# Optimization experiments

Measured on AMD Instinct MI355X. Metric: run time of the kernel, lower is better.

Reference implementation:

```python
import jax, jax.numpy as jnp
import numpy as np
from itertools import combinations_with_replacement

B, T, F, L, POLY_ORDER = 16, 2048, 128, 16, 3


def _hilbert_filter(N):
    # Matches pytorch_hilbert: H[0]=0, H[1:N//2]=2, H[N//2]=0 (even N)
    h = np.zeros(N, dtype=np.float32)
    if N % 2 == 0:
        h[1:N // 2] = 2.0
    else:
        h[1:(N + 1) // 2] = 2.0
    return jnp.asarray(h)


def hilbert(sig, axis=1):
    N = sig.shape[axis]
    Xf = jnp.fft.fft(sig, axis=axis)
    shape = [1] * sig.ndim
    shape[axis] = N
    return jnp.fft.ifft(Xf * _hilbert_filter(N).reshape(shape), axis=axis)


def _combo_indices(latent, poly_order):
    # static index arrays, grouped by degree n
    return [np.array(list(combinations_with_replacement(range(latent), n)), dtype=np.int32)
            for n in range(1, poly_order + 1)]


def compute_library(z, poly_order):
    # z: [B, T, L] -> theta: [B, T, library_dim]
    feats = []
    for combos in _combo_indices(z.shape[-1], poly_order):
        zc = z[..., combos]            # [B, T, ncomb, n]
        feats.append(jnp.prod(zc, axis=-1))  # [B, T, ncomb]
    analytic = hilbert(z, axis=1)
    feats.append(z)
    feats.append(jnp.abs(analytic))    # extract_real_component
    feats.append(jnp.angle(analytic))  # extract_imaginary_component
    return jnp.concatenate(feats, axis=-1)


def setup_inputs() -> dict:
    key = jax.random.key(0)
    ks = jax.random.split(key, 7)
    lib_dim = L + 2 * L + sum(len(c) for c in _combo_indices(L, POLY_ORDER))
    s_enc = 1.0 / np.sqrt(F)
    s_dec = 1.0 / np.sqrt(L)
    s_sin = 1.0 / np.sqrt(lib_dim)
    return {
        "x": jax.random.normal(ks[0], (B, T, F), dtype=jnp.float32),
        "W_enc": jax.random.uniform(ks[1], (L, F), jnp.float32, -s_enc, s_enc),
        "b_enc": jax.random.uniform(ks[2], (L,), jnp.float32, -s_enc, s_enc),
        "W_dec": jax.random.uniform(ks[3], (F, L), jnp.float32, -s_dec, s_dec),
        "b_dec": jax.random.uniform(ks[4], (F,), jnp.float32, -s_dec, s_dec),
        "W_sindy": jax.random.uniform(ks[5], (L, lib_dim), jnp.float32, -s_sin, s_sin),
        "b_sindy": jax.random.uniform(ks[6], (L,), jnp.float32, -s_sin, s_sin),
    }


def reference(x, W_enc, b_enc, W_dec, b_dec, W_sindy, b_sindy):
    z = jnp.einsum('btf,lf->btl', x, W_enc) + b_enc          # encoder
    theta = compute_library(z, POLY_ORDER)                    # [B,T,lib_dim]
    y_hat = jnp.einsum('btd,ld->btl', theta, W_sindy) + b_sindy
    x_hat = jnp.einsum('btl,fl->btf', z, W_dec) + b_dec       # decoder
    # Jacobian of the linear encoder w.r.t. x is the constant weight matrix
    # broadcast per (b, t): identical math to the O((B*T)^2) autograd version.
    jac_z_x = jnp.broadcast_to(W_enc, (x.shape[0], x.shape[1], L, F))
    return (y_hat, x_hat, z, jac_z_x, W_sindy, W_dec)
```

## Files before the change

kernel.cpp:

```cpp
#include <hip/hip_runtime.h>
#include <math.h>

typedef unsigned short u16;
typedef unsigned int   u32;
typedef __attribute__((ext_vector_type(4))) float f32x4;

#define OFF_AT    0
#define OFF_PT    524288
#define OFF_WT    1048576
#define OFF_ZT    1064832
#define OFF_TWC   1589120
#define OFF_TWS   1591168

#define R1_LO 0
#define R1_HI 5592576
#define R2_LO 5592576
#define R2_HI 11185152
#define R3_LO 11185152
#define R3_HI 16777216

__device__ __forceinline__ void jac_range(const float* __restrict__ Wenc,
                                          float* __restrict__ out_jac,
                                          int lo, int hi, int idx, int nth)
{
    const float* wsrc = Wenc + (size_t)((lo + idx) & 511) * 4;
    f32x4 w;
    w.x = wsrc[0]; w.y = wsrc[1]; w.z = wsrc[2]; w.w = wsrc[3];
    f32x4* j4 = (f32x4*)out_jac;
    for (int i = lo + idx; i < hi; i += nth)
        __builtin_nontemporal_store(w, j4 + i);
}

__global__ __launch_bounds__(256) void k1_encdec(
    const float* __restrict__ x, const float* __restrict__ Wenc, const float* __restrict__ benc,
    const float* __restrict__ Wdec, const float* __restrict__ bdec,
    const float* __restrict__ Wsin,
    float* __restrict__ out_z, float* __restrict__ out_xhat,
    float* __restrict__ out_Ws, float* __restrict__ out_Wd,
    float* __restrict__ z_t, float* __restrict__ wt,
    double* __restrict__ twc_g, double* __restrict__ tws_g,
    float* __restrict__ out_jac)
{
    int tid = threadIdx.x;
    int blk = blockIdx.x;

    if (blk >= 2116) {
        jac_range(Wenc, out_jac, R1_LO, R1_HI, (blk - 2116) * 256 + tid, 262144);
        return;
    }
    if (blk >= 2048) {
        int t0 = (blk - 2048) * 256 + tid;
        if (t0 < 16256) {
            float v = Wsin[t0];
            out_Ws[t0] = v;
            int l = t0 / 1016;
            int d = t0 - l * 1016;
            if (d < 16) v += Wsin[t0 + 968];
            wt[d * 16 + l] = v;
        } else if (t0 < 17280) {
            int k = t0 - 16256;
            double ang = -6.283185307179586476925286766559 * (double)k / 2048.0;
            double s_, c_;
            sincos(ang, &s_, &c_);
            twc_g[k] = c_;
            tws_g[k] = s_;
        }
        if (t0 < 2048) out_Wd[t0] = Wdec[t0];
        return;
    }

    __shared__ float xs[16][128];
    __shared__ float we[16][132];
    __shared__ float wd[128][17];
    __shared__ float zs[16][16];

    {
        const float4* xv = (const float4*)x + (size_t)blk * 512;
        float* dst = &xs[0][0];
        float4 a = xv[tid], b = xv[tid + 256];
        dst[tid*4+0]=a.x; dst[tid*4+1]=a.y; dst[tid*4+2]=a.z; dst[tid*4+3]=a.w;
        dst[(tid+256)*4+0]=b.x; dst[(tid+256)*4+1]=b.y; dst[(tid+256)*4+2]=b.z; dst[(tid+256)*4+3]=b.w;
    }
    {
        const float4* wev = (const float4*)Wenc;
        #pragma unroll
        for (int h = 0; h < 2; ++h) {
            int vi = tid + h * 256;
            float4 v = wev[vi];
            int base = vi * 4, row = base >> 7, col = base & 127;
            we[row][col+0]=v.x; we[row][col+1]=v.y; we[row][col+2]=v.z; we[row][col+3]=v.w;
        }
    }
    {
        const float4* wdv = (const float4*)Wdec;
        #pragma unroll
        for (int h = 0; h < 2; ++h) {
            int vi = tid + h * 256;
            float4 v = wdv[vi];
            int base = vi * 4, row = base >> 4, col = base & 15;
            wd[row][col+0]=v.x; wd[row][col+1]=v.y; wd[row][col+2]=v.z; wd[row][col+3]=v.w;
        }
    }
    __syncthreads();

    {
        int r = tid >> 4, l = tid & 15;
        float s = 0.f;
        #pragma unroll 8
        for (int f = 0; f < 128; ++f) s += xs[r][f] * we[l][f];
        float zv = s + benc[l];
        zs[r][l] = zv;
        out_z[blk * 256 + tid] = zv;
    }
    __syncthreads();

    {
        int l2 = tid >> 4, r2 = tid & 15;
        z_t[l2 * 32768 + blk * 16 + r2] = zs[r2][l2];
    }

    #pragma unroll
    for (int u = 0; u < 8; ++u) {
        int idx = u * 256 + tid;
        int rr = idx >> 7, f = idx & 127;
        float acc = bdec[f];
        #pragma unroll
        for (int ll = 0; ll < 16; ++ll) acc += zs[rr][ll] * wd[f][ll];
        out_xhat[(size_t)blk * 2048 + idx] = acc;
    }
}

#define TWPAD(k) ((k) + ((k) >> 5))
#define CP(i)    ((i) + ((i) >> 4))

__global__ __launch_bounds__(1024) void k2_hilbert(
    const float* __restrict__ z_t, const double* __restrict__ twc_g,
    const double* __restrict__ tws_g, const float* __restrict__ Wenc,
    float* __restrict__ a_t, float* __restrict__ p_t,
    float* __restrict__ out_jac)
{
    __shared__ double2 c[2176];
    __shared__ double twc_s[1056];
    __shared__ double tws_s[1056];

    int tid = threadIdx.x;
    if (blockIdx.x >= 256) {
        jac_range(Wenc, out_jac, R2_LO, R2_HI, (blockIdx.x - 256) * 1024 + tid, 524288);
        return;
    }
    int b = blockIdx.x >> 4, l = blockIdx.x & 15;
    const size_t base = (size_t)l * 32768 + (size_t)b * 2048;
    const float* zp = z_t + base;

    {
        twc_s[TWPAD(tid)] = twc_g[tid];
        tws_s[TWPAD(tid)] = tws_g[tid];
    }
    {
        double2 v0; v0.x = (double)zp[tid];        v0.y = 0.0;
        double2 v1; v1.x = (double)zp[tid + 1024]; v1.y = 0.0;
        c[CP(tid)] = v0;
        c[CP(tid + 1024)] = v1;
    }
    __syncthreads();

    for (int half = 1024; half >= 1; half >>= 1) {
        int step = 1024 / half;
        int j = tid & (half - 1);
        int pos = ((tid - j) << 1) + j;
        int pa = CP(pos), pb = CP(pos + half);
        int ti = TWPAD(j * step);
        double2 u = c[pa], v = c[pb];
        double wc = twc_s[ti], wsn = tws_s[ti];
        double2 s, dsc;
        s.x = u.x + v.x;  s.y = u.y + v.y;
        double br = u.x - v.x, bi = u.y - v.y;
        dsc.x = br * wc - bi * wsn;
        dsc.y = br * wsn + bi * wc;
        c[pa] = s;
        c[pb] = dsc;
        __syncthreads();
    }

    #pragma unroll
    for (int h = 0; h < 2; ++h) {
        int t = tid + h * 1024;
        double sc = (t == 0 || (t & 1)) ? 0.0 : (2.0 / 2048.0);
        int ci = CP(t);
        double2 v = c[ci];
        v.x *= sc; v.y *= sc;
        c[ci] = v;
    }
    __syncthreads();

    for (int half = 1; half <= 1024; half <<= 1) {
        int step = 1024 / half;
        int j = tid & (half - 1);
        int pos = ((tid - j) << 1) + j;
        int pa = CP(pos), pb = CP(pos + half);
        int ti = TWPAD(j * step);
        double2 u = c[pa], v = c[pb];
        double wc = twc_s[ti], wsn = tws_s[ti];
        double tr = v.x * wc + v.y * wsn;
        double ti2 = v.y * wc - v.x * wsn;
        double2 p0, p1;
        p0.x = u.x + tr; p0.y = u.y + ti2;
        p1.x = u.x - tr; p1.y = u.y - ti2;
        c[pa] = p0;
        c[pb] = p1;
        __syncthreads();
    }

    #pragma unroll
    for (int h = 0; h < 2; ++h) {
        int t = tid + h * 1024;
        double2 v = c[CP(t)];
        a_t[base + t] = (float)sqrt(v.x * v.x + v.y * v.y);
        p_t[base + t] = (float)atan2(v.y, v.x);
    }
}

#define EMIT2(EXPR) do {                                                    \
    if ((unsigned)(d - LO) < 121u) {                                        \
        float vv[2];                                                        \
        _Pragma("unroll") for (int p = 0; p < 2; ++p) vv[p] = (EXPR);       \
        int bb = (d - LO) << 4;                                             \
        _Pragma("unroll") for (int l = 0; l < 16; ++l) {                    \
            float w = lw[bb + l];                                           \
            acc[0][l] = fmaf(vv[0], w, acc[0][l]);                          \
            acc[1][l] = fmaf(vv[1], w, acc[1][l]);                          \
        }                                                                   \
    }                                                                       \
    ++d;                                                                    \
} while (0)

template<int LO>
__device__ __forceinline__ void poly_accum(const float (&z)[2][16],
                                           const float* __restrict__ lw,
                                           float (&acc)[2][16])
{
    int d = 0;
    #pragma unroll
    for (int i = 0; i < 16; ++i) EMIT2(z[p][i]);
    #pragma unroll
    for (int i = 0; i < 16; ++i)
        #pragma unroll
        for (int j = i; j < 16; ++j) EMIT2(z[p][i] * z[p][j]);
    #pragma unroll
    for (int i = 0; i < 16; ++i)
        #pragma unroll
        for (int j = i; j < 16; ++j)
            #pragma unroll
            for (int k = j; k < 16; ++k) EMIT2(z[p][i] * z[p][j] * z[p][k]);
}

__global__ __launch_bounds__(256, 2) void k3_yhat(
    const float* __restrict__ z_ws, const float* __restrict__ wt,
    const float* __restrict__ Wenc,
    float* __restrict__ part, float* __restrict__ out_jac)
{
    __shared__ float lw[1936];
    int tid = threadIdx.x;
    if (blockIdx.x >= 512) {
        jac_range(Wenc, out_jac, R3_LO, R3_HI, (blockIdx.x - 512) * 256 + tid, 262144);
        return;
    }
    int slice = blockIdx.x >> 6;
    int ptgrp = blockIdx.x & 63;
    int base = ptgrp * 512;

    {
        const float4* src = (const float4*)(wt + slice * 121 * 16);
        float4* dst = (float4*)lw;
        for (int i = tid; i < 484; i += 256) dst[i] = src[i];
    }
    __syncthreads();

    float z[2][16], acc[2][16];
    #pragma unroll
    for (int p = 0; p < 2; ++p) {
        int bt = base + p * 256 + tid;
        const float4* zp = (const float4*)(z_ws + (size_t)bt * 16);
        #pragma unroll
        for (int q = 0; q < 4; ++q) {
            float4 v = zp[q];
            z[p][q*4+0]=v.x; z[p][q*4+1]=v.y; z[p][q*4+2]=v.z; z[p][q*4+3]=v.w;
        }
    }
    #pragma unroll
    for (int p = 0; p < 2; ++p)
        #pragma unroll
        for (int l = 0; l < 16; ++l) acc[p][l] = 0.f;

    switch (slice) {
        case 0: poly_accum<0 * 121>(z, lw, acc); break;
        case 1: poly_accum<1 * 121>(z, lw, acc); break;
        case 2: poly_accum<2 * 121>(z, lw, acc); break;
        case 3: poly_accum<3 * 121>(z, lw, acc); break;
        case 4: poly_accum<4 * 121>(z, lw, acc); break;
        case 5: poly_accum<5 * 121>(z, lw, acc); break;
        case 6: poly_accum<6 * 121>(z, lw, acc); break;
        default: poly_accum<7 * 121>(z, lw, acc); break;
    }

    #pragma unroll
    for (int p = 0; p < 2; ++p) {
        int bt = base + p * 256 + tid;
        float4* pp = (float4*)(part + (size_t)slice * 524288 + (size_t)bt * 16);
        #pragma unroll
        for (int q = 0; q < 4; ++q) {
            float4 v;
            v.x = acc[p][q*4+0]; v.y = acc[p][q*4+1];
            v.z = acc[p][q*4+2]; v.w = acc[p][q*4+3];
            pp[q] = v;
        }
    }
}

__global__ __launch_bounds__(256) void k3_tail(
    const float* __restrict__ part, const float* __restrict__ a_t,
    const float* __restrict__ p_t, const float* __restrict__ wt,
    const float* __restrict__ bsin, float* __restrict__ out_y)
{
    __shared__ float lw[512];
    int tid = threadIdx.x;
    if (tid < 128) {
        ((float4*)lw)[tid] = ((const float4*)(wt + 984 * 16))[tid];
    }
    __syncthreads();

    int bt = blockIdx.x * 128 + (tid >> 1);
    int lh = (tid & 1) * 8;
    float acc[8];
    {
        const float4* bp = (const float4*)bsin;
        #pragma unroll
        for (int q = 0; q < 2; ++q) {
            float4 v = bp[(lh >> 2) + q];
            acc[q*4+0]=v.x; acc[q*4+1]=v.y; acc[q*4+2]=v.z; acc[q*4+3]=v.w;
        }
    }
    #pragma unroll
    for (int sl = 0; sl < 8; ++sl) {
        const float4* pp = (const float4*)(part + (size_t)sl * 524288 + (size_t)bt * 16 + lh);
        #pragma unroll
        for (int q = 0; q < 2; ++q) {
            float4 v = pp[q];
            acc[q*4+0]+=v.x; acc[q*4+1]+=v.y; acc[q*4+2]+=v.z; acc[q*4+3]+=v.w;
        }
    }
    #pragma unroll
    for (int i = 0; i < 16; ++i) {
        float av = a_t[(size_t)i * 32768 + bt];
        #pragma unroll
        for (int l = 0; l < 8; ++l) acc[l] = fmaf(av, lw[i * 16 + lh + l], acc[l]);
    }
    #pragma unroll
    for (int i = 0; i < 16; ++i) {
        float pv = p_t[(size_t)i * 32768 + bt];
        #pragma unroll
        for (int l = 0; l < 8; ++l) acc[l] = fmaf(pv, lw[256 + i * 16 + lh + l], acc[l]);
    }

    float4* yp = (float4*)(out_y + (size_t)bt * 16 + lh);
    #pragma unroll
    for (int q = 0; q < 2; ++q) {
        float4 v;
        v.x = acc[q*4+0]; v.y = acc[q*4+1]; v.z = acc[q*4+2]; v.w = acc[q*4+3];
        yp[q] = v;
    }
}

extern "C" void kernel_launch(void* const* d_in, const int* in_sizes, int n_in,
                              void* d_out, int out_size, void* d_ws, size_t ws_size,
                              hipStream_t stream)
{
    const float* x  = (const float*)d_in[0];
    const float* We = (const float*)d_in[1];
    const float* be = (const float*)d_in[2];
    const float* Wd = (const float*)d_in[3];
    const float* bd = (const float*)d_in[4];
    const float* Ws = (const float*)d_in[5];
    const float* bs = (const float*)d_in[6];

    float* out  = (float*)d_out;
    float* o_y  = out;
    float* o_xh = out + 524288;
    float* o_z  = out + 4718592;
    float* o_j  = out + 5242880;
    float* o_Ws = out + 72351744;
    float* o_Wd = out + 72368000;

    float*  ws    = (float*)d_ws;
    float*  a_t   = ws + OFF_AT;
    float*  p_t   = ws + OFF_PT;
    float*  wt    = ws + OFF_WT;
    float*  z_t   = ws + OFF_ZT;
    double* twc_g = (double*)(ws + OFF_TWC);
    double* tws_g = (double*)(ws + OFF_TWS);
    float*  part  = ws + 1593216;

    hipLaunchKernelGGL(k1_encdec, dim3(3140), dim3(256), 0, stream,
                       x, We, be, Wd, bd, Ws, o_z, o_xh, o_Ws, o_Wd,
                       z_t, wt, twc_g, tws_g, o_j);
    hipLaunchKernelGGL(k2_hilbert, dim3(768), dim3(1024), 0, stream,
                       z_t, twc_g, tws_g, We, a_t, p_t, o_j);
    hipLaunchKernelGGL(k3_yhat, dim3(1536), dim3(256), 0, stream,
                       o_z, wt, We, part, o_j);
    hipLaunchKernelGGL(k3_tail, dim3(256), dim3(256), 0, stream,
                       part, a_t, p_t, wt, bs, o_y);
}
```

Before: 331.8 us.

## Process 32 timesteps per encoder block with vectorized LDS and register-held decoder weights

Measured after the change: 329.1 us, median of 2. No clear change (-0.8%).

```diff
diff --git a/kernel.cpp b/kernel.cpp
--- a/kernel.cpp
+++ b/kernel.cpp
@@ -44,12 +44,12 @@
     int tid = threadIdx.x;
     int blk = blockIdx.x;
 
-    if (blk >= 2116) {
-        jac_range(Wenc, out_jac, R1_LO, R1_HI, (blk - 2116) * 256 + tid, 262144);
+    if (blk >= 1092) {
+        jac_range(Wenc, out_jac, R1_LO, R1_HI, (blk - 1092) * 256 + tid, 262144);
         return;
     }
-    if (blk >= 2048) {
-        int t0 = (blk - 2048) * 256 + tid;
+    if (blk >= 1024) {
+        int t0 = (blk - 1024) * 256 + tid;
         if (t0 < 16256) {
             float v = Wsin[t0];
             out_Ws[t0] = v;
@@ -69,26 +69,29 @@
         return;
     }
 
-    __shared__ float xs[16][128];
+    __shared__ float xs[32][132];
     __shared__ float we[16][132];
-    __shared__ float wd[128][17];
-    __shared__ float zs[16][16];
-
-    {
-        const float4* xv = (const float4*)x + (size_t)blk * 512;
-        float* dst = &xs[0][0];
-        float4 a = xv[tid], b = xv[tid + 256];
-        dst[tid*4+0]=a.x; dst[tid*4+1]=a.y; dst[tid*4+2]=a.z; dst[tid*4+3]=a.w;
-        dst[(tid+256)*4+0]=b.x; dst[(tid+256)*4+1]=b.y; dst[(tid+256)*4+2]=b.z; dst[(tid+256)*4+3]=b.w;
+    __shared__ float wdT[16][132];
+    __shared__ float zs[32][20];
+
+    {
+        const float4* xv = (const float4*)x + (size_t)blk * 1024;
+        float4* xs4 = (float4*)&xs[0][0];
+        #pragma unroll
+        for (int h = 0; h < 4; ++h) {
+            int vi = tid + h * 256;
+            int pt = vi >> 5, fq = vi & 31;
+            xs4[pt * 33 + fq] = xv[vi];
+        }
     }
     {
         const float4* wev = (const float4*)Wenc;
+        float4* we4 = (float4*)&we[0][0];
         #pragma unroll
         for (int h = 0; h < 2; ++h) {
             int vi = tid + h * 256;
-            float4 v = wev[vi];
-            int base = vi * 4, row = base >> 7, col = base & 127;
-            we[row][col+0]=v.x; we[row][col+1]=v.y; we[row][col+2]=v.z; we[row][col+3]=v.w;
+            int l = vi >> 5, fq = vi & 31;
+            we4[l * 33 + fq] = wev[vi];
         }
     }
     {
@@ -97,36 +100,68 @@
         for (int h = 0; h < 2; ++h) {
             int vi = tid + h * 256;
             float4 v = wdv[vi];
-            int base = vi * 4, row = base >> 4, col = base & 15;
-            wd[row][col+0]=v.x; wd[row][col+1]=v.y; wd[row][col+2]=v.z; wd[row][col+3]=v.w;
-        }
-    }
-    __syncthreads();
-
-    {
-        int r = tid >> 4, l = tid & 15;
-        float s = 0.f;
+            int f = vi >> 2, lq = (vi & 3) * 4;
+            wdT[lq + 0][f] = v.x; wdT[lq + 1][f] = v.y;
+            wdT[lq + 2][f] = v.z; wdT[lq + 3][f] = v.w;
+        }
+    }
+    __syncthreads();
+
+    {
+        int pt = tid >> 3, lp = tid & 7;
+        const float4* xr = (const float4*)&xs[pt][0];
+        const float4* wa = (const float4*)&we[lp][0];
+        const float4* wb = (const float4*)&we[lp + 8][0];
+        float s0 = 0.f, s1 = 0.f;
         #pragma unroll 8
-        for (int f = 0; f < 128; ++f) s += xs[r][f] * we[l][f];
-        float zv = s + benc[l];
-        zs[r][l] = zv;
-        out_z[blk * 256 + tid] = zv;
-    }
-    __syncthreads();
-
-    {
-        int l2 = tid >> 4, r2 = tid & 15;
-        z_t[l2 * 32768 + blk * 16 + r2] = zs[r2][l2];
-    }
-
-    #pragma unroll
-    for (int u = 0; u < 8; ++u) {
-        int idx = u * 256 + tid;
-        int rr = idx >> 7, f = idx & 127;
-        float acc = bdec[f];
-        #pragma unroll
-        for (int ll = 0; ll < 16; ++ll) acc += zs[rr][ll] * wd[f][ll];
-        out_xhat[(size_t)blk * 2048 + idx] = acc;
+        for (int fq = 0; fq < 32; ++fq) {
+            float4 a = xr[fq], u = wa[fq], v = wb[fq];
+            s0 = fmaf(a.x, u.x, s0); s0 = fmaf(a.y, u.y, s0);
+            s0 = fmaf(a.z, u.z, s0); s0 = fmaf(a.w, u.w, s0);
+            s1 = fmaf(a.x, v.x, s1); s1 = fmaf(a.y, v.y, s1);
+            s1 = fmaf(a.z, v.z, s1); s1 = fmaf(a.w, v.w, s1);
+        }
+        zs[pt][lp]     = s0 + benc[lp];
+        zs[pt][lp + 8] = s1 + benc[lp + 8];
+    }
+    __syncthreads();
+
+    {
+        #pragma unroll
+        for (int h = 0; h < 2; ++h) {
+            int i = tid + h * 256;
+            out_z[(size_t)blk * 512 + i] = zs[i >> 4][i & 15];
+        }
+        #pragma unroll
+        for (int h = 0; h < 2; ++h) {
+            int i = tid + h * 256;
+            int l = i >> 5, pt = i & 31;
+            z_t[(size_t)l * 32768 + blk * 32 + pt] = zs[pt][l];
+        }
+    }
+
+    {
+        int f = tid & 127, half = tid >> 7;
+        float w[16];
+        #pragma unroll
+        for (int l = 0; l < 16; ++l) w[l] = wdT[l][f];
+        float bd = bdec[f];
+        #pragma unroll
+        for (int p = 0; p < 16; ++p) {
+            int pt = half * 16 + p;
+            const float4* zr = (const float4*)&zs[pt][0];
+            float4 z0 = zr[0], z1 = zr[1], z2 = zr[2], z3 = zr[3];
+            float acc = bd;
+            acc = fmaf(z0.x, w[0],  acc); acc = fmaf(z0.y, w[1],  acc);
+            acc = fmaf(z0.z, w[2],  acc); acc = fmaf(z0.w, w[3],  acc);
+            acc = fmaf(z1.x, w[4],  acc); acc = fmaf(z1.y, w[5],  acc);
+            acc = fmaf(z1.z, w[6],  acc); acc = fmaf(z1.w, w[7],  acc);
+            acc = fmaf(z2.x, w[8],  acc); acc = fmaf(z2.y, w[9],  acc);
+            acc = fmaf(z2.z, w[10], acc); acc = fmaf(z2.w, w[11], acc);
+            acc = fmaf(z3.x, w[12], acc); acc = fmaf(z3.y, w[13], acc);
+            acc = fmaf(z3.z, w[14], acc); acc = fmaf(z3.w, w[15], acc);
+            out_xhat[(size_t)blk * 4096 + (size_t)pt * 128 + f] = acc;
+        }
     }
 }
 
@@ -400,7 +435,7 @@
     double* tws_g = (double*)(ws + OFF_TWS);
     float*  part  = ws + 1593216;
 
-    hipLaunchKernelGGL(k1_encdec, dim3(3140), dim3(256), 0, stream,
+    hipLaunchKernelGGL(k1_encdec, dim3(2116), dim3(256), 0, stream,
                        x, We, be, Wd, bd, Ws, o_z, o_xh, o_Ws, o_Wd,
                        z_t, wt, twc_g, tws_g, o_j);
     hipLaunchKernelGGL(k2_hilbert, dim3(768), dim3(1024), 0, stream,
```
